# Kernel tuning notes

Hardware: AMD Instinct MI355X
Metric: run time of the kernel (lower is better)

## Reference

```python
import jax, jax.numpy as jnp
import numpy as np

N_NODES = 50000
N_EDGES = 800000
SLOPE = 0.2
DIMS = [(256, 256), (256, 256), (256, 256), (256, 256), (256, 256), (256, 128)]


def gcn_conv(x, W, b, src, dst, dinv):
    # x: [N, in], W: [out, in], b: [out]
    h = x @ W.T  # [N, out]
    norm = dinv[src] * dinv[dst]  # [E]
    msg = h[src] * norm[:, None]  # [E, out]
    agg = jax.ops.segment_sum(msg, dst, num_segments=N_NODES)
    # self-loop contribution: norm_ii = dinv[i]^2
    agg = agg + h * (dinv * dinv)[:, None]
    return agg + b


def setup_inputs() -> dict:
    key = jax.random.key(0)
    ks = jax.random.split(key, 2 + 2 * len(DIMS))
    inp = {
        "x": jax.random.normal(ks[0], (N_NODES, 256), dtype=jnp.float32),
        "edge_index": jax.random.randint(ks[1], (2, N_EDGES), 0, N_NODES, dtype=jnp.int64)
        if jax.config.read("jax_enable_x64")
        else jax.random.randint(ks[1], (2, N_EDGES), 0, N_NODES, dtype=jnp.int32),
    }
    for i, (din, dout) in enumerate(DIMS):
        inp[f"w{i+1}"] = jax.random.normal(ks[2 + 2 * i], (dout, din), dtype=jnp.float32) / np.sqrt(din)
        inp[f"b{i+1}"] = jax.random.normal(ks[3 + 2 * i], (dout,), dtype=jnp.float32) * 0.01
    return inp


def reference(x, edge_index, w1, b1, w2, b2, w3, b3, w4, b4, w5, b5, w6, b6):
    src, dst = edge_index[0], edge_index[1]
    # symmetric normalization with self-loops: deg_i = 1 + sum of incoming edges
    deg = jax.ops.segment_sum(jnp.ones_like(src, dtype=x.dtype), dst, num_segments=N_NODES) + 1.0
    dinv = jax.lax.rsqrt(deg)

    def lrelu(h):
        return jnp.where(h >= 0, h, SLOPE * h)

    h = gcn_conv(x, w1, b1, src, dst, dinv)
    for W, b in [(w2, b2), (w3, b3), (w4, b4), (w5, b5)]:
        h = gcn_conv(lrelu(h), W, b, src, dst, dinv)
    h = gcn_conv(lrelu(h), w6, b6, src, dst, dinv)
    return h
```

## Files before the change

kernel.cpp:

```cpp
#include <hip/hip_runtime.h>
#include <hip/hip_bf16.h>

#define K_DIM 256
__device__ __forceinline__ float lrelu_f(float x) { return x >= 0.f ? x : 0.2f * x; }

using bf16x8 = __attribute__((ext_vector_type(8))) short;
using f32x4 = __attribute__((ext_vector_type(4))) float;

__device__ __forceinline__ unsigned short f2bf(float x) {
  __hip_bfloat16 b = __float2bfloat16(x);
  return *(unsigned short*)&b;
}
__device__ __forceinline__ float bf2f(unsigned short u) {
  __hip_bfloat16 b = *(__hip_bfloat16*)&u;
  return __bfloat162float(b);
}


__global__ __launch_bounds__(256) void hist_kernel(const int* __restrict__ dst,
                                                   int* __restrict__ cnt, int E) {
  int e = blockIdx.x * 256 + threadIdx.x;
  if (e < E) atomicAdd(&cnt[dst[e]], 1);
}

__global__ __launch_bounds__(256) void dinv_kernel(const int* __restrict__ cnt,
                                                   float* __restrict__ dinv, int n) {
  int i = blockIdx.x * 256 + threadIdx.x;
  if (i < n) dinv[i] = rsqrtf((float)cnt[i] + 1.0f);
}

__global__ __launch_bounds__(256) void scan1_kernel(const int* __restrict__ cnt,
                                                    int* __restrict__ incl,
                                                    int* __restrict__ bsum, int n) {
  __shared__ int sm[256];
  int t = threadIdx.x;
  int i = blockIdx.x * 256 + t;
  int v = (i < n) ? cnt[i] : 0;
  sm[t] = v;
  __syncthreads();
  for (int off = 1; off < 256; off <<= 1) {
    int u = (t >= off) ? sm[t - off] : 0;
    __syncthreads();
    sm[t] += u;
    __syncthreads();
  }
  if (i < n) incl[i] = sm[t];
  if (t == 255) bsum[blockIdx.x] = sm[255];
}

__global__ __launch_bounds__(256) void scan2_kernel(const int* __restrict__ bsum,
                                                    int* __restrict__ boff, int nb) {
  __shared__ int sm[256];
  int t = threadIdx.x;
  int v = (t < nb) ? bsum[t] : 0;
  sm[t] = v;
  __syncthreads();
  for (int off = 1; off < 256; off <<= 1) {
    int u = (t >= off) ? sm[t - off] : 0;
    __syncthreads();
    sm[t] += u;
    __syncthreads();
  }
  boff[t] = sm[t] - v;
}

__global__ __launch_bounds__(256) void scan3_kernel(const int* __restrict__ incl,
                                                    const int* __restrict__ boff,
                                                    int* __restrict__ rowptr, int n) {
  int i = blockIdx.x * 256 + threadIdx.x;
  if (i < n) rowptr[i + 1] = incl[i] + boff[blockIdx.x];
  if (i == 0) rowptr[0] = 0;
}

__global__ __launch_bounds__(256) void scatter_kernel(const int* __restrict__ src,
                                                      const int* __restrict__ dst,
                                                      const int* __restrict__ rowptr,
                                                      int* __restrict__ cursor,
                                                      const float* __restrict__ dinv,
                                                      int* __restrict__ esrc,
                                                      float* __restrict__ ew, int E) {
  int e = blockIdx.x * 256 + threadIdx.x;
  if (e < E) {
    int d = dst[e];
    int p = rowptr[d] + atomicAdd(&cursor[d], 1);
    int s = src[e];
    esrc[p] = s;
    ew[p] = dinv[s];
  }
}


template <bool LRELU>
__global__ __launch_bounds__(256) void split_kernel(const float* __restrict__ in,
                                                    unsigned short* __restrict__ hi,
                                                    unsigned short* __restrict__ lo,
                                                    int n4) {
  int i = blockIdx.x * 256 + threadIdx.x;
  if (i >= n4) return;
  float4 v = *(const float4*)(in + (size_t)i * 4);
  if (LRELU) {
    v.x = lrelu_f(v.x); v.y = lrelu_f(v.y); v.z = lrelu_f(v.z); v.w = lrelu_f(v.w);
  }
  ushort4 h, l;
  h.x = f2bf(v.x); l.x = f2bf(v.x - bf2f(h.x));
  h.y = f2bf(v.y); l.y = f2bf(v.y - bf2f(h.y));
  h.z = f2bf(v.z); l.z = f2bf(v.z - bf2f(h.z));
  h.w = f2bf(v.w); l.w = f2bf(v.w - bf2f(h.w));
  *(ushort4*)(hi + (size_t)i * 4) = h;
  *(ushort4*)(lo + (size_t)i * 4) = l;
}


template <int NCOLS>
__global__ __launch_bounds__(256) void mfma_gemm_kernel(
    const unsigned short* __restrict__ Ah, const unsigned short* __restrict__ Al,
    const unsigned short* __restrict__ Wh, const unsigned short* __restrict__ Wl,
    float* __restrict__ H, int M) {
  constexpr int NY = NCOLS / 64;
  const int bx = blockIdx.x / NY;
  const int by = blockIdx.x % NY;
  const int tid = threadIdx.x;
  const int wv = tid >> 6;
  const int lane = tid & 63;
  const int r = lane & 15;
  const int g = lane >> 4;
  const int bm = bx * 256 + wv * 64;
  const int bn = by * 64;

  f32x4 acc[4][4];
#pragma unroll
  for (int i = 0; i < 4; ++i)
#pragma unroll
    for (int t = 0; t < 4; ++t) acc[i][t] = {0.f, 0.f, 0.f, 0.f};

  size_t aoff[4];
#pragma unroll
  for (int i = 0; i < 4; ++i) {
    int row = bm + i * 16 + r;
    if (row >= M) row = M - 1;
    aoff[i] = (size_t)row * K_DIM;
  }
  size_t woff[4];
#pragma unroll
  for (int t = 0; t < 4; ++t) woff[t] = (size_t)(bn + t * 16 + r) * K_DIM;

  for (int k0 = 0; k0 < K_DIM; k0 += 32) {
    const int kb = k0 + g * 8;
    bf16x8 ah[4], al[4], bh[4], bl[4];
#pragma unroll
    for (int i = 0; i < 4; ++i) {
      ah[i] = *(const bf16x8*)(Ah + aoff[i] + kb);
      al[i] = *(const bf16x8*)(Al + aoff[i] + kb);
    }
#pragma unroll
    for (int t = 0; t < 4; ++t) {
      bh[t] = *(const bf16x8*)(Wh + woff[t] + kb);
      bl[t] = *(const bf16x8*)(Wl + woff[t] + kb);
    }
#pragma unroll
    for (int i = 0; i < 4; ++i)
#pragma unroll
      for (int t = 0; t < 4; ++t) {
        acc[i][t] = __builtin_amdgcn_mfma_f32_16x16x32_bf16(ah[i], bh[t], acc[i][t], 0, 0, 0);
        acc[i][t] = __builtin_amdgcn_mfma_f32_16x16x32_bf16(ah[i], bl[t], acc[i][t], 0, 0, 0);
        acc[i][t] = __builtin_amdgcn_mfma_f32_16x16x32_bf16(al[i], bh[t], acc[i][t], 0, 0, 0);
      }
  }

#pragma unroll
  for (int i = 0; i < 4; ++i)
#pragma unroll
    for (int t = 0; t < 4; ++t) {
#pragma unroll
      for (int j = 0; j < 4; ++j) {
        int row = bm + i * 16 + g * 4 + j;
        if (row < M) H[(size_t)row * NCOLS + bn + t * 16 + r] = acc[i][t][j];
      }
    }
}


template <int COLS, bool FUSE>
__global__ __launch_bounds__(256) void aggregate_kernel(
    const float* __restrict__ H, const int* __restrict__ rowptr,
    const int* __restrict__ esrc, const float* __restrict__ ew,
    const float* __restrict__ dinv, const float* __restrict__ bias,
    float* __restrict__ out, unsigned short* __restrict__ oh,
    unsigned short* __restrict__ ol, int n) {
  constexpr int CW = COLS / 8;
  constexpr int TPN = CW / 4;
  constexpr int NPB = 256 / TPN;
  const int g = blockIdx.x & 7;
  const int nb = blockIdx.x >> 3;
  const int t = threadIdx.x;
  const int ln = t / TPN;
  const int ct = t % TPN;
  const int node = nb * NPB + ln;
  if (node >= n) return;
  const int c0 = g * CW + ct * 4;
  const float* __restrict__ Hc = H + c0;
  const float di = dinv[node];

  float4 hs = *(const float4*)(Hc + (size_t)node * COLS);
  float a0 = di * hs.x, a1 = di * hs.y, a2 = di * hs.z, a3 = di * hs.w;

  const int e1 = rowptr[node + 1];
  int e = rowptr[node];
  for (; e + 4 <= e1; e += 4) {
    int s0 = esrc[e + 0], s1 = esrc[e + 1], s2 = esrc[e + 2], s3 = esrc[e + 3];
    float w0 = ew[e + 0], w1 = ew[e + 1], w2 = ew[e + 2], w3 = ew[e + 3];
    float4 h0 = *(const float4*)(Hc + (size_t)s0 * COLS);
    float4 h1 = *(const float4*)(Hc + (size_t)s1 * COLS);
    float4 h2 = *(const float4*)(Hc + (size_t)s2 * COLS);
    float4 h3 = *(const float4*)(Hc + (size_t)s3 * COLS);
    a0 = fmaf(w3, h3.x, fmaf(w2, h2.x, fmaf(w1, h1.x, fmaf(w0, h0.x, a0))));
    a1 = fmaf(w3, h3.y, fmaf(w2, h2.y, fmaf(w1, h1.y, fmaf(w0, h0.y, a1))));
    a2 = fmaf(w3, h3.z, fmaf(w2, h2.z, fmaf(w1, h1.z, fmaf(w0, h0.z, a2))));
    a3 = fmaf(w3, h3.w, fmaf(w2, h2.w, fmaf(w1, h1.w, fmaf(w0, h0.w, a3))));
  }
  for (; e < e1; ++e) {
    int s = esrc[e];
    float w = ew[e];
    float4 h = *(const float4*)(Hc + (size_t)s * COLS);
    a0 = fmaf(w, h.x, a0);
    a1 = fmaf(w, h.y, a1);
    a2 = fmaf(w, h.z, a2);
    a3 = fmaf(w, h.w, a3);
  }

  float4 b = *(const float4*)(bias + c0);
  float o0 = fmaf(di, a0, b.x);
  float o1 = fmaf(di, a1, b.y);
  float o2 = fmaf(di, a2, b.z);
  float o3 = fmaf(di, a3, b.w);

  if constexpr (FUSE) {
    o0 = lrelu_f(o0); o1 = lrelu_f(o1); o2 = lrelu_f(o2); o3 = lrelu_f(o3);
    ushort4 h, l;
    h.x = f2bf(o0); l.x = f2bf(o0 - bf2f(h.x));
    h.y = f2bf(o1); l.y = f2bf(o1 - bf2f(h.y));
    h.z = f2bf(o2); l.z = f2bf(o2 - bf2f(h.z));
    h.w = f2bf(o3); l.w = f2bf(o3 - bf2f(h.w));
    *(ushort4*)(oh + (size_t)node * COLS + c0) = h;
    *(ushort4*)(ol + (size_t)node * COLS + c0) = l;
  } else {
    float4 o;
    o.x = o0; o.y = o1; o.z = o2; o.w = o3;
    *(float4*)(out + (size_t)node * COLS + c0) = o;
  }
}


extern "C" void kernel_launch(void* const* d_in, const int* in_sizes, int n_in,
                              void* d_out, int out_size, void* d_ws, size_t ws_size,
                              hipStream_t stream) {
  (void)n_in; (void)out_size; (void)ws_size;
  const float* x = (const float*)d_in[0];
  const int N = in_sizes[0] / 256;
  const int* ei = (const int*)d_in[1];
  const int E = in_sizes[1] / 2;
  const int* srcp = ei;
  const int* dstp = ei + E;
  const float* Wl6[6];
  const float* Bl[6];
  for (int i = 0; i < 6; i++) {
    Wl6[i] = (const float*)d_in[2 + 2 * i];
    Bl[i] = (const float*)d_in[3 + 2 * i];
  }
  float* out = (float*)d_out;

  char* p = (char*)d_ws;
  auto carve = [&](size_t bytes) {
    char* r = p;
    p += (bytes + 255) & ~(size_t)255;
    return (void*)r;
  };
  const int Mpad = (N + 255) & ~255;
  float* bufB = (float*)carve((size_t)N * 256 * 4);
  unsigned short* ah = (unsigned short*)carve((size_t)Mpad * 256 * 2);
  unsigned short* al = (unsigned short*)carve((size_t)Mpad * 256 * 2);
  unsigned short* wh = (unsigned short*)carve((size_t)256 * 256 * 2);
  unsigned short* wl = (unsigned short*)carve((size_t)256 * 256 * 2);
  int* cnt = (int*)carve((size_t)N * 4);
  float* dinv = (float*)carve((size_t)N * 4);
  int* incl = (int*)carve((size_t)N * 4);
  int* rowptr = (int*)carve((size_t)(N + 1) * 4);
  int* esrc = (int*)carve((size_t)E * 4);
  float* ew = (float*)carve((size_t)E * 4);
  int* bsum = (int*)carve(1024);
  int* boff = (int*)carve(1024);

  const int NB = (N + 255) / 256;

  hipMemsetAsync(cnt, 0, (size_t)N * 4, stream);
  hist_kernel<<<(E + 255) / 256, 256, 0, stream>>>(dstp, cnt, E);
  dinv_kernel<<<NB, 256, 0, stream>>>(cnt, dinv, N);
  scan1_kernel<<<NB, 256, 0, stream>>>(cnt, incl, bsum, N);
  scan2_kernel<<<1, 256, 0, stream>>>(bsum, boff, NB);
  scan3_kernel<<<NB, 256, 0, stream>>>(incl, boff, rowptr, N);
  hipMemsetAsync(cnt, 0, (size_t)N * 4, stream);
  scatter_kernel<<<(E + 255) / 256, 256, 0, stream>>>(srcp, dstp, rowptr, cnt, dinv,
                                                      esrc, ew, E);

  const int n4 = N * 64;
  const int gsplit = (n4 + 255) / 256;
  const int gmfma_x = (N + 255) / 256;
  const int gagg256 = 8 * ((N + 31) / 32);
  const int gagg128 = 8 * ((N + 63) / 64);

  split_kernel<false><<<gsplit, 256, 0, stream>>>(x, ah, al, n4);
  split_kernel<false><<<(256 * 64 + 255) / 256, 256, 0, stream>>>(Wl6[0], wh, wl, 256 * 64);
  mfma_gemm_kernel<256><<<gmfma_x * 4, 256, 0, stream>>>(ah, al, wh, wl, bufB, N);
  aggregate_kernel<256, true><<<gagg256, 256, 0, stream>>>(bufB, rowptr, esrc, ew, dinv,
                                                           Bl[0], nullptr, ah, al, N);
  for (int l = 1; l < 5; ++l) {
    split_kernel<false><<<(256 * 64 + 255) / 256, 256, 0, stream>>>(Wl6[l], wh, wl, 256 * 64);
    mfma_gemm_kernel<256><<<gmfma_x * 4, 256, 0, stream>>>(ah, al, wh, wl, bufB, N);
    aggregate_kernel<256, true><<<gagg256, 256, 0, stream>>>(bufB, rowptr, esrc, ew, dinv,
                                                             Bl[l], nullptr, ah, al, N);
  }
  split_kernel<false><<<(128 * 64 + 255) / 256, 256, 0, stream>>>(Wl6[5], wh, wl, 128 * 64);
  mfma_gemm_kernel<128><<<gmfma_x * 2, 256, 0, stream>>>(ah, al, wh, wl, bufB, N);
  aggregate_kernel<128, false><<<gagg128, 256, 0, stream>>>(bufB, rowptr, esrc, ew, dinv,
                                                            Bl[5], out, nullptr, nullptr, N);
}
```

Measured before the change: 1.105 ms.

## Store bf16 activation and weight splits in MFMA fragment-tiled layout

Split and aggregate kernels now write bf16 hi/lo operands in a fragment-major tiled layout, so each GEMM wave loads a contiguous 16-byte-per-lane fragment instead of strided row reads. This is meant to make the MFMA GEMM's global loads fully coalesced. A zero-tail kernel pads the A buffers up to a padded row count, and the grid now covers the padded rows. It relies on Mpad being defined in the hidden launch code and adds scattered writes in the producers.

```diff
diff --git a/kernel.cpp b/kernel.cpp
--- a/kernel.cpp
+++ b/kernel.cpp
@@ -14,6 +14,11 @@
 __device__ __forceinline__ float bf2f(unsigned short u) {
   __hip_bfloat16 b = *(__hip_bfloat16*)&u;
   return __bfloat162float(b);
+}
+
+__device__ __forceinline__ size_t frag_idx(int row, int k) {
+  return (((size_t)(row >> 4) * 8 + (k >> 5)) * 64 + (row & 15) + (((k >> 3) & 3) << 4)) * 8 +
+         (k & 7);
 }
 
 
@@ -89,6 +94,16 @@
   }
 }
 
+__global__ __launch_bounds__(256) void zerotail_kernel(unsigned short* __restrict__ a,
+                                                       unsigned short* __restrict__ b,
+                                                       size_t start, size_t count) {
+  size_t i = (size_t)blockIdx.x * 256 + threadIdx.x;
+  if (i < count) {
+    a[start + i] = 0;
+    b[start + i] = 0;
+  }
+}
+
 
 template <bool LRELU>
 __global__ __launch_bounds__(256) void split_kernel(const float* __restrict__ in,
@@ -97,7 +112,10 @@
                                                     int n4) {
   int i = blockIdx.x * 256 + threadIdx.x;
   if (i >= n4) return;
-  float4 v = *(const float4*)(in + (size_t)i * 4);
+  int flat = i * 4;
+  int row = flat >> 8;
+  int k = flat & 255;
+  float4 v = *(const float4*)(in + (size_t)flat);
   if (LRELU) {
     v.x = lrelu_f(v.x); v.y = lrelu_f(v.y); v.z = lrelu_f(v.z); v.w = lrelu_f(v.w);
   }
@@ -106,8 +124,9 @@
   h.y = f2bf(v.y); l.y = f2bf(v.y - bf2f(h.y));
   h.z = f2bf(v.z); l.z = f2bf(v.z - bf2f(h.z));
   h.w = f2bf(v.w); l.w = f2bf(v.w - bf2f(h.w));
-  *(ushort4*)(hi + (size_t)i * 4) = h;
-  *(ushort4*)(lo + (size_t)i * 4) = l;
+  size_t d = frag_idx(row, k);
+  *(ushort4*)(hi + d) = h;
+  *(ushort4*)(lo + d) = l;
 }
 
 
@@ -133,29 +152,22 @@
 #pragma unroll
     for (int t = 0; t < 4; ++t) acc[i][t] = {0.f, 0.f, 0.f, 0.f};
 
-  size_t aoff[4];
-#pragma unroll
-  for (int i = 0; i < 4; ++i) {
-    int row = bm + i * 16 + r;
-    if (row >= M) row = M - 1;
-    aoff[i] = (size_t)row * K_DIM;
-  }
-  size_t woff[4];
-#pragma unroll
-  for (int t = 0; t < 4; ++t) woff[t] = (size_t)(bn + t * 16 + r) * K_DIM;
-
-  for (int k0 = 0; k0 < K_DIM; k0 += 32) {
-    const int kb = k0 + g * 8;
+  const int tm0 = bm >> 4;
+  const int tn0 = bn >> 4;
+
+  for (int tk = 0; tk < 8; ++tk) {
     bf16x8 ah[4], al[4], bh[4], bl[4];
 #pragma unroll
     for (int i = 0; i < 4; ++i) {
-      ah[i] = *(const bf16x8*)(Ah + aoff[i] + kb);
-      al[i] = *(const bf16x8*)(Al + aoff[i] + kb);
+      size_t base = (((size_t)(tm0 + i) * 8 + tk) * 64) * 8 + (size_t)lane * 8;
+      ah[i] = *(const bf16x8*)(Ah + base);
+      al[i] = *(const bf16x8*)(Al + base);
     }
 #pragma unroll
     for (int t = 0; t < 4; ++t) {
-      bh[t] = *(const bf16x8*)(Wh + woff[t] + kb);
-      bl[t] = *(const bf16x8*)(Wl + woff[t] + kb);
+      size_t base = (((size_t)(tn0 + t) * 8 + tk) * 64) * 8 + (size_t)lane * 8;
+      bh[t] = *(const bf16x8*)(Wh + base);
+      bl[t] = *(const bf16x8*)(Wl + base);
     }
 #pragma unroll
     for (int i = 0; i < 4; ++i)
@@ -241,8 +253,9 @@
     h.y = f2bf(o1); l.y = f2bf(o1 - bf2f(h.y));
     h.z = f2bf(o2); l.z = f2bf(o2 - bf2f(h.z));
     h.w = f2bf(o3); l.w = f2bf(o3 - bf2f(h.w));
-    *(ushort4*)(oh + (size_t)node * COLS + c0) = h;
-    *(ushort4*)(ol + (size_t)node * COLS + c0) = l;
+    size_t d = frag_idx(node, c0);
+    *(ushort4*)(oh + d) = h;
+    *(ushort4*)(ol + d) = l;
   } else {
     float4 o;
     o.x = o0; o.y = o1; o.z = o2; o.w = o3;
@@ -301,10 +314,16 @@
   hipMemsetAsync(cnt, 0, (size_t)N * 4, stream);
   scatter_kernel<<<(E + 255) / 256, 256, 0, stream>>>(srcp, dstp, rowptr, cnt, dinv,
                                                       esrc, ew, E);
+  {
+    size_t start = (size_t)(N / 16) * 8 * 64 * 8;
+    size_t total = (size_t)(Mpad / 16) * 8 * 64 * 8;
+    size_t count = total - start;
+    zerotail_kernel<<<(int)((count + 255) / 256), 256, 0, stream>>>(ah, al, start, count);
+  }
 
   const int n4 = N * 64;
   const int gsplit = (n4 + 255) / 256;
-  const int gmfma_x = (N + 255) / 256;
+  const int gmfma_x = Mpad / 256;
   const int gagg256 = 8 * ((N + 31) / 32);
   const int gagg128 = 8 * ((N + 63) / 64);
 
```

Result: faster. 937.7 us (-15.2%).
